# Optimization experiments

Hardware: AMD Instinct MI355X
Metric: run time of the kernel (lower is better)

## Reference

```python
import jax, jax.numpy as jnp
import numpy as np
import math

B, S, D, H, DFF = 4, 2048, 1024, 16, 4096
DK = D // 2  # 512; per-head dim = DK // H = 32
LN_EPS = 1e-3  # keras LayerNormalization default


def gelu_tanh(x):
    c = math.sqrt(2.0 / math.pi)
    return 0.5 * x * (1.0 + jnp.tanh(c * (x + 0.044715 * x * x * x)))


def layer_norm(z, g, b):
    mu = jnp.mean(z, axis=-1, keepdims=True)
    var = jnp.mean(jnp.square(z - mu), axis=-1, keepdims=True)
    return (z - mu) * jax.lax.rsqrt(var + LN_EPS) * g + b


def setup_inputs() -> dict:
    key = jax.random.key(0)
    ks = jax.random.split(key, 10)
    s = 0.02
    return {
        "x": jax.random.normal(ks[0], (B, S, D), dtype=jnp.float32),
        "mask": jnp.zeros((1, 1, S, S), dtype=jnp.float32),
        "Wq": jax.random.normal(ks[1], (D, DK), dtype=jnp.float32) * s,
        "bq": jnp.zeros((DK,), jnp.float32),
        "Wk": jax.random.normal(ks[2], (D, DK), dtype=jnp.float32) * s,
        "bk": jnp.zeros((DK,), jnp.float32),
        "Wv": jax.random.normal(ks[3], (D, DK), dtype=jnp.float32) * s,
        "bv": jnp.zeros((DK,), jnp.float32),
        "Wo": jax.random.normal(ks[4], (DK, D), dtype=jnp.float32) * s,
        "bo": jnp.zeros((D,), jnp.float32),
        "W1": jax.random.normal(ks[5], (D, DFF), dtype=jnp.float32) * s,
        "b1": jnp.zeros((DFF,), jnp.float32),
        "W2": jax.random.normal(ks[6], (DFF, D), dtype=jnp.float32) * s,
        "b2": jnp.zeros((D,), jnp.float32),
        "g1": jnp.ones((D,), jnp.float32),
        "be1": jnp.zeros((D,), jnp.float32),
        "g2": jnp.ones((D,), jnp.float32),
        "be2": jnp.zeros((D,), jnp.float32),
    }


def reference(x, mask, Wq, bq, Wk, bk, Wv, bv, Wo, bo, W1, b1, W2, b2, g1, be1, g2, be2):
    dh = DK // H
    # QKV projections: D -> DK total, split over H heads
    q = (x @ Wq + bq).reshape(B, S, H, dh).transpose(0, 2, 1, 3)  # [B,H,S,dh]
    k = (x @ Wk + bk).reshape(B, S, H, dh).transpose(0, 2, 1, 3)
    v = (x @ Wv + bv).reshape(B, S, H, dh).transpose(0, 2, 1, 3)
    # NOTE: source scales by sqrt(d_k)=sqrt(DK), not per-head dim
    scores = jnp.einsum("bhqd,bhkd->bhqk", q, k) / jnp.sqrt(jnp.asarray(DK, x.dtype))
    scores = scores + (-1e9) * mask
    w = jax.nn.softmax(scores, axis=-1)
    o = jnp.einsum("bhqk,bhkd->bhqd", w, v)  # [B,H,S,dh]
    o = o.transpose(0, 2, 1, 3).reshape(B, S, DK)
    attn_out = o @ Wo + bo  # [B,S,D]
    h1 = layer_norm(x + attn_out, g1, be1)
    # NOTE: source applies GELU AFTER the second Dense
    ff = gelu_tanh((h1 @ W1 + b1) @ W2 + b2)
    return layer_norm(h1 + ff, g2, be2)
```

## Files before the change

### kernel.cpp

```cpp
#include <hip/hip_runtime.h>

typedef unsigned short u16;
typedef unsigned int   u32;
typedef short s16x8 __attribute__((ext_vector_type(8)));
typedef float f32x4 __attribute__((ext_vector_type(4)));
typedef s16x8 __attribute__((may_alias)) s16x8_a;
typedef f32x4 __attribute__((may_alias)) f32x4_a;

#define S_LEN   2048
#define D_MODEL 1024
#define DK_DIM  512
#define DFF_DIM 4096
#define MS_ROWS 8192

__device__ __forceinline__ u16 f2bf(float f) {
  union { float f; unsigned u; } x; x.f = f;
  unsigned r = x.u + 0x7fffu + ((x.u >> 16) & 1u);
  return (u16)(r >> 16);
}
__device__ __forceinline__ float bf2f(u16 u) {
  union { unsigned u; float f; } x; x.u = ((unsigned)u) << 16; return x.f;
}

__device__ __forceinline__ void gload_lds16(const void* g, void* l) {
  __builtin_amdgcn_global_load_lds(
      (const __attribute__((address_space(1))) unsigned int*)g,
      (__attribute__((address_space(3))) unsigned int*)l, 16, 0, 0);
}


__global__ __launch_bounds__(256)
void cast_f32_bf16(const float* __restrict__ in, u16* __restrict__ out, int n) {
  for (int i = (blockIdx.x * 256 + threadIdx.x) * 4; i < n; i += gridDim.x * 256 * 4) {
    float4 f = *(const float4*)&in[i];
    ushort4 u;
    u.x = f2bf(f.x); u.y = f2bf(f.y); u.z = f2bf(f.z); u.w = f2bf(f.w);
    *(ushort4*)&out[i] = u;
  }
}

__global__ __launch_bounds__(256)
void cast_transpose_t(const float* __restrict__ W, u16* __restrict__ Wt, int K, int N) {
  __shared__ float T[64][65];
  const int k0 = blockIdx.x * 64, n0 = blockIdx.y * 64;
  const int tr = threadIdx.x >> 4;
  const int tc = (threadIdx.x & 15) * 4;
#pragma unroll
  for (int i = 0; i < 4; i++) {
    float4 v = *(const float4*)&W[(size_t)(k0 + tr + i * 16) * N + n0 + tc];
    T[tr + i * 16][tc + 0] = v.x; T[tr + i * 16][tc + 1] = v.y;
    T[tr + i * 16][tc + 2] = v.z; T[tr + i * 16][tc + 3] = v.w;
  }
  __syncthreads();
#pragma unroll
  for (int i = 0; i < 4; i++) {
    int nrow = tr + i * 16;
    ushort4 u;
    u.x = f2bf(T[tc + 0][nrow]); u.y = f2bf(T[tc + 1][nrow]);
    u.z = f2bf(T[tc + 2][nrow]); u.w = f2bf(T[tc + 3][nrow]);
    *(ushort4*)&Wt[(size_t)(n0 + nrow) * K + k0 + tc] = u;
  }
}

__global__ __launch_bounds__(256)
void fill0(float* __restrict__ p, int n) {
  int i = blockIdx.x * 256 + threadIdx.x;
  if (i < n) p[i] = 0.f;
}

__global__ __launch_bounds__(256)
void wct_reduce(const float* __restrict__ wctp, u16* __restrict__ wct) {
  int i = (blockIdx.x * 256 + threadIdx.x) * 4;
  float4 s = *(const float4*)&wctp[i];
#pragma unroll
  for (int p = 1; p < 8; p++) {
    float4 v = *(const float4*)&wctp[(size_t)p * 1048576 + i];
    s.x += v.x; s.y += v.y; s.z += v.z; s.w += v.w;
  }
  ushort4 u;
  u.x = f2bf(s.x); u.y = f2bf(s.y); u.z = f2bf(s.z); u.w = f2bf(s.w);
  *(ushort4*)&wct[i] = u;
}

__global__ __launch_bounds__(64)
void bc_make(const float* __restrict__ b1, const float* __restrict__ b2,
             const u16* __restrict__ w2t, float* __restrict__ bc) {
  int n = blockIdx.x, l = threadIdx.x;
  float s = 0.f;
  for (int d = l * 8; d < DFF_DIM; d += 64 * 8) {
    s16x8 v = *(const s16x8_a*)&w2t[(size_t)n * DFF_DIM + d];
#pragma unroll
    for (int j = 0; j < 8; j++) s += b1[d + j] * bf2f((u16)v[j]);
  }
#pragma unroll
  for (int o = 32; o > 0; o >>= 1) s += __shfl_down(s, o, 64);
  if (l == 0) bc[n] = s + b2[n];
}


template<int BM, int TBN, int OMODE>
__global__ __launch_bounds__(512, 2)
void gemm8(const u16* __restrict__ A, const u16* __restrict__ Bt,
           const float* __restrict__ b1p, const float* __restrict__ b2p,
           const float* __restrict__ b3p,
           float* __restrict__ Cf, u16* __restrict__ Cb,
           u16* __restrict__ Ck, u16* __restrict__ Cv,
           int M, int N, int K)
{
  constexpr int NF = TBN / 64;
  constexpr int MF = BM / 32;
  constexpr int MFP = MF / 4;
  constexpr int LA = BM / 128;
  constexpr int LB = TBN / 128;
  constexpr int AHROWS = BM / 2;
  constexpr int BHROWS = TBN / 2;
  constexpr int AH_U = AHROWS * 64;
  constexpr int SLOT_B0 = BM * 64;
  constexpr int BUFU = BM * 64 + TBN * 64;
  __shared__ __align__(16) u16 lds[2 * BUFU];

  const int tid = threadIdx.x;
  const int l = tid & 63, w = tid >> 6;
  const int wrow = w >> 2, wcol = w & 3;
  const int fr = l & 15, g = l >> 4;

  const int nxt = N / TBN;
  const int nwg = gridDim.x;
  const int wg = (blockIdx.x & 7) * (nwg >> 3) + (blockIdx.x >> 3);
  const int n0 = (wg % nxt) * TBN;
  const int m0 = (wg / nxt) * BM;

  const int NT = K / 64;
  const int NITER = NT / 2;

  const int srow = l >> 3;
  const int sgc  = (l & 7) ^ srow;
  auto stageA = [&](int buf, int part, int kt) {
#pragma unroll
    for (int i = 0; i < LA; i++) {
      int row = i * 64 + w * 8 + srow;
      gload_lds16(A + (size_t)(m0 + part * AHROWS + row) * K + kt * 64 + sgc * 8,
                  (void*)&lds[buf * BUFU + part * AH_U + (i * 512 + w * 64) * 8]);
    }
  };
  auto stageB = [&](int buf, int part, int kt) {
#pragma unroll
    for (int i = 0; i < LB; i++) {
      int row = i * 64 + w * 8 + srow;
      gload_lds16(Bt + (size_t)(n0 + part * BHROWS + row) * K + kt * 64 + sgc * 8,
                  (void*)&lds[buf * BUFU + SLOT_B0 + part * (TBN * 32) + (i * 512 + w * 64) * 8]);
    }
  };

  f32x4 acc[MF][NF];
#pragma unroll
  for (int m = 0; m < MF; m++)
#pragma unroll
    for (int n = 0; n < NF; n++)
#pragma unroll
      for (int r = 0; r < 4; r++) acc[m][n][r] = 0.f;
  s16x8 bfrag[NF][2];

  stageA(0, 0, 0); stageA(0, 1, 0); stageB(0, 0, 0); stageB(0, 1, 0);
  stageB(1, 0, 1); stageB(1, 1, 1);
  if (LB == 2) asm volatile("s_waitcnt vmcnt(4)" ::: "memory");
  else         asm volatile("s_waitcnt vmcnt(2)" ::: "memory");
  __builtin_amdgcn_s_barrier();

  auto phase = [&](int buf, int q, auto stager, int vm) {
    s16x8 afr[MFP][2];
    const int abase = buf * BUFU + wrow * AH_U;
#pragma unroll
    for (int f2 = 0; f2 < MFP; f2++)
#pragma unroll
      for (int kk = 0; kk < 2; kk++)
        afr[f2][kk] = *(const s16x8_a*)
            &lds[abase + ((q * MFP + f2) * 16 + fr) * 64 + (((kk * 4 + g) ^ (fr & 7)) * 8)];
    if (q == 0) {
      const int bbase = buf * BUFU + SLOT_B0 + (wcol >> 1) * (TBN * 32) + (wcol & 1) * ((TBN / 4) * 64);
#pragma unroll
      for (int n = 0; n < NF; n++)
#pragma unroll
        for (int kk = 0; kk < 2; kk++)
          bfrag[n][kk] = *(const s16x8_a*)
              &lds[bbase + (n * 16 + fr) * 64 + (((kk * 4 + g) ^ (fr & 7)) * 8)];
    }
    stager();
    if (q == 0)
      asm volatile("s_waitcnt lgkmcnt(8)" ::: "memory");
    __builtin_amdgcn_s_barrier();
    asm volatile("s_waitcnt lgkmcnt(0)" ::: "memory");
    __builtin_amdgcn_sched_barrier(0);
    __builtin_amdgcn_s_setprio(1);
#pragma unroll
    for (int f2 = 0; f2 < MFP; f2++)
#pragma unroll
      for (int n = 0; n < NF; n++)
#pragma unroll
        for (int kk = 0; kk < 2; kk++)
          acc[q * MFP + f2][n] = __builtin_amdgcn_mfma_f32_16x16x32_bf16(
              afr[f2][kk], bfrag[n][kk], acc[q * MFP + f2][n], 0, 0, 0);
    __builtin_amdgcn_s_setprio(0);
    if (vm == 0)      asm volatile("s_waitcnt vmcnt(0)" ::: "memory");
    else if (vm == 2) asm volatile("s_waitcnt vmcnt(2)" ::: "memory");
    else if (vm == 4) asm volatile("s_waitcnt vmcnt(4)" ::: "memory");
    __builtin_amdgcn_s_barrier();
  };

  for (int j = 0; j < NITER; ++j) {
    const int t1 = 2 * j + 1;
    const bool more = (j + 1 < NITER);
    phase(0, 0, [&]{ stageA(1, 0, t1); }, -1);
    phase(0, 1, [&]{ stageA(1, 1, t1); }, -1);
    phase(0, 2, [&]{ if (more) stageB(0, 0, t1 + 1); }, -1);
    phase(0, 3, [&]{ if (more) stageB(0, 1, t1 + 1); }, more ? 2 * LB : 0);
    phase(1, 0, [&]{ if (more) stageA(0, 0, t1 + 1); }, -1);
    phase(1, 1, [&]{ if (more) stageA(0, 1, t1 + 1); }, -1);
    phase(1, 2, [&]{ if (more) stageB(1, 0, t1 + 2); }, -1);
    phase(1, 3, [&]{ if (more) stageB(1, 1, t1 + 2); }, more ? 2 * LB : -1);
  }

  const int rb = m0 + wrow * AHROWS + g * 4;
  const int cb = n0 + wcol * (TBN / 4) + fr;
#pragma unroll
  for (int m = 0; m < MF; m++) {
#pragma unroll
    for (int n = 0; n < NF; n++) {
      const int col = cb + n * 16;
      const int row0 = rb + m * 16;
      if (OMODE == 0) {
        float bz = b1p[col];
#pragma unroll
        for (int r = 0; r < 4; r++)
          Cb[(size_t)(row0 + r) * N + col] = f2bf(acc[m][n][r] + bz);
      } else if (OMODE == 1) {
        float bz = b1p[col];
#pragma unroll
        for (int r = 0; r < 4; r++)
          Cf[(size_t)(row0 + r) * N + col] = acc[m][n][r] + bz;
      } else {
        if (col < 512) {
          float bz = b1p[col];
#pragma unroll
          for (int r = 0; r < 4; r++)
            Cb[(size_t)(row0 + r) * 512 + col] = f2bf(acc[m][n][r] + bz);
        } else if (col < 1024) {
          float bz = b2p[col - 512];
#pragma unroll
          for (int r = 0; r < 4; r++)
            Ck[(size_t)(row0 + r) * 512 + (col - 512)] = f2bf(acc[m][n][r] + bz);
        } else {
          float bz = b3p[col - 1024];
          const int cv = col - 1024;
          const int bb = row0 >> 11, ss = row0 & 2047;
          const int hd = cv >> 5, dd = cv & 31;
          ushort4 u4;
          u4.x = f2bf(acc[m][n][0] + bz);
          u4.y = f2bf(acc[m][n][1] + bz);
          u4.z = f2bf(acc[m][n][2] + bz);
          u4.w = f2bf(acc[m][n][3] + bz);
          *(ushort4*)&Cv[((size_t)(bb * 16 + hd) * 32 + dd) * 2048 + ss] = u4;
        }
      }
    }
  }
}


template<int OMODE, bool TRIBIAS>
__global__ __launch_bounds__(512, 4)
void gemmT(const u16* __restrict__ A, const u16* __restrict__ Bt,
           const float* __restrict__ b1p, const float* __restrict__ b2p,
           const float* __restrict__ b3p,
           float* __restrict__ Cf, u16* __restrict__ Cb,
           int M, int N, int Kblk, int lda, long partStride)
{
  __shared__ __align__(16) u16 lds[3 * 12288];

  const int tid = threadIdx.x;
  const int l = tid & 63, w = tid >> 6;
  const int wrow = w >> 2, wcol = w & 3;
  const int fr = l & 15, g = l >> 4;

  const int nxt = N >> 8;
  const int nwg = gridDim.x;
  const int wg = (blockIdx.x & 7) * (nwg >> 3) + (blockIdx.x >> 3);
  const int n0 = (wg % nxt) * 256;
  const int m0 = (wg / nxt) * 128;
  const long koff = (long)blockIdx.y * Kblk;

  const int NT = Kblk >> 5;

  const int srow = l >> 2;
  const int sck  = (l & 3) ^ ((l >> 3) & 3);
  auto stage = [&](int kt, int bi) {
    const long kb = koff + kt * 32 + sck * 8;
    gload_lds16(A + (size_t)(m0 + w * 16 + srow) * lda + kb,
                (void*)&lds[bi * 12288 + w * 512]);
    gload_lds16(Bt + (size_t)(n0 + w * 16 + srow) * lda + kb,
                (void*)&lds[bi * 12288 + 4096 + w * 512]);
    gload_lds16(Bt + (size_t)(n0 + 128 + w * 16 + srow) * lda + kb,
                (void*)&lds[bi * 12288 + 8192 + w * 512]);
  };

  f32x4 acc[4][4];
#pragma unroll
  for (int m = 0; m < 4; m++)
#pragma unroll
    for (int n = 0; n < 4; n++)
#pragma unroll
      for (int r = 0; r < 4; r++) acc[m][n][r] = 0.f;

  stage(0, 0);
  stage(1, 1);
  asm volatile("s_waitcnt vmcnt(3)" ::: "memory");
  __builtin_amdgcn_s_barrier();

  const int rsw = (g ^ ((fr >> 1) & 3)) * 8;
  int bi = 0;
  for (int t = 0; t < NT; ++t) {
    s16x8 afr[4], bfr[4];
    const int ab = bi * 12288 + fr * 32 + rsw;
#pragma unroll
    for (int m = 0; m < 4; m++)
      afr[m] = *(const s16x8_a*)&lds[ab + (wrow * 64 + m * 16) * 32];
#pragma unroll
    for (int n = 0; n < 4; n++)
      bfr[n] = *(const s16x8_a*)&lds[ab + 4096 + (wcol * 64 + n * 16) * 32];
    const bool more2 = (t + 2 < NT);
    if (more2) {
      int b2i = bi + 2; if (b2i >= 3) b2i -= 3;
      stage(t + 2, b2i);
    }
    asm volatile("s_waitcnt lgkmcnt(0)" ::: "memory");
    __builtin_amdgcn_sched_barrier(0);
    __builtin_amdgcn_s_setprio(1);
#pragma unroll
    for (int m = 0; m < 4; m++)
#pragma unroll
      for (int n = 0; n < 4; n++)
        acc[m][n] = __builtin_amdgcn_mfma_f32_16x16x32_bf16(afr[m], bfr[n], acc[m][n], 0, 0, 0);
    __builtin_amdgcn_s_setprio(0);
    if (more2)            asm volatile("s_waitcnt vmcnt(3)" ::: "memory");
    else if (t + 1 < NT)  asm volatile("s_waitcnt vmcnt(0)" ::: "memory");
    __builtin_amdgcn_s_barrier();
    bi = (bi + 1 == 3) ? 0 : bi + 1;
  }

  float* ldsf = (float*)lds;
  const bool dobias = (blockIdx.y == 0);
#pragma unroll
  for (int p = 0; p < 2; p++) {
    if (p) __syncthreads();
    const int wb = w * 2180;
#pragma unroll
    for (int j = 0; j < 2; j++)
#pragma unroll
      for (int n = 0; n < 4; n++)
#pragma unroll
        for (int r = 0; r < 4; r++)
          ldsf[wb + (j * 16 + g * 4 + r) * 68 + n * 16 + fr] = acc[2 * p + j][n][r];
    __syncthreads();
#pragma unroll
    for (int i = 0; i < 8; i++) {
      int lin = i * 512 + tid;
      int rl = lin >> 6, ch = lin & 63;
      int row_g = m0 + 32 * p + (rl & 31) + (rl >> 5) * 64;
      int colbase = n0 + ch * 4;
      const float* src = &ldsf[((rl >> 5) * 4 + (ch >> 4)) * 2180 + (rl & 31) * 68 + (ch & 15) * 4];
      f32x4 v = *(const f32x4_a*)src;
      if (dobias) {
        const float* bp;
        int cb2;
        if (TRIBIAS) {
          bp = colbase < 512 ? b1p : (colbase < 1024 ? b2p : b3p);
          cb2 = colbase & 511;
        } else { bp = b1p; cb2 = colbase; }
        float4 bz = *(const float4*)&bp[cb2];
        v[0] += bz.x; v[1] += bz.y; v[2] += bz.z; v[3] += bz.w;
      }
      if (OMODE == 1) {
        *(float4*)&Cf[(size_t)row_g * N + colbase + blockIdx.y * partStride] =
            *(float4*)&v;
      } else {
        ushort4 u;
        u.x = f2bf(v[0]); u.y = f2bf(v[1]); u.z = f2bf(v[2]); u.w = f2bf(v[3]);
        *(ushort4*)&Cb[(size_t)row_g * N + colbase] = u;
      }
    }
  }
}


__global__ __launch_bounds__(256, 4)
void flash_attn(const u16* __restrict__ q, const u16* __restrict__ k,
                const u16* __restrict__ vt, u16* __restrict__ o)
{
  __shared__ __align__(16) u16 Ks[64 * 32];
  __shared__ __align__(16) u16 Vts[32 * 72];
  __shared__ __align__(16) u32 Ps[4 * 16 * 36];
  const int tid = threadIdx.x;
  const int l = tid & 63, w = tid >> 6;
  const int fr = l & 15, g = l >> 4;
  const int fk = g * 8;
  const int bh = blockIdx.y;
  const int b = bh >> 4, head = bh & 15;
  const int s0 = blockIdx.x * 128;
  const size_t qk_base = (size_t)b * S_LEN * DK_DIM + (size_t)head * 32;
  const size_t vt_base = (size_t)bh * 32 * S_LEN;

  s16x8 qf[2];
#pragma unroll
  for (int hh = 0; hh < 2; hh++)
    qf[hh] = *(const s16x8_a*)&q[qk_base + (size_t)(s0 + w * 32 + hh * 16 + fr) * DK_DIM + fk];

  f32x4 oacc[2][2];
#pragma unroll
  for (int hh = 0; hh < 2; hh++)
#pragma unroll
    for (int nb = 0; nb < 2; nb++)
#pragma unroll
      for (int r = 0; r < 4; r++) oacc[hh][nb][r] = 0.f;
  float lsum[2] = {0.f, 0.f};

  const float kScale = 0.044194173824159216f;

  const int kc_row = w * 16 + (l >> 2);
  const int kc_col = (l & 3) * 8;
  const int vd = tid >> 3;
  const int vc = tid & 7;
  const int wbase = w * 576;

  for (int kb = 0; kb < S_LEN; kb += 64) {
    gload_lds16(&k[qk_base + (size_t)(kb + kc_row) * DK_DIM + kc_col], (void*)&Ks[w * 512]);
    {
      s16x8 vv = *(const s16x8_a*)&vt[vt_base + (size_t)vd * S_LEN + kb + vc * 8];
      *(s16x8_a*)&Vts[vd * 72 + vc * 8] = vv;
    }
    __syncthreads();

    s16x8 af[4], vf[2][2];
#pragma unroll
    for (int nb = 0; nb < 4; nb++)
      af[nb] = *(const s16x8_a*)&Ks[(nb * 16 + fr) * 32 + fk];
#pragma unroll
    for (int kk = 0; kk < 2; kk++)
#pragma unroll
      for (int nb = 0; nb < 2; nb++)
        vf[kk][nb] = *(const s16x8_a*)&Vts[(nb * 16 + fr) * 72 + kk * 32 + fk];

#pragma unroll
    for (int hh = 0; hh < 2; hh++) {
      f32x4 sc[4];
#pragma unroll
      for (int nb = 0; nb < 4; nb++) {
        f32x4 z; z[0] = 0.f; z[1] = 0.f; z[2] = 0.f; z[3] = 0.f;
        sc[nb] = __builtin_amdgcn_mfma_f32_16x16x32_bf16(af[nb], qf[hh], z, 0, 0, 0);
      }
      float ls = 0.f;
#pragma unroll
      for (int nb = 0; nb < 4; nb++)
#pragma unroll
        for (int r = 0; r < 4; r++) {
          float p = __expf(sc[nb][r] * kScale);
          sc[nb][r] = p; ls += p;
        }
      lsum[hh] += ls;
#pragma unroll
      for (int nb = 0; nb < 4; nb++) {
        u32 pk0, pk1;
        asm("v_cvt_pk_bf16_f32 %0, %1, %2" : "=v"(pk0) : "v"(sc[nb][0]), "v"(sc[nb][1]));
        asm("v_cvt_pk_bf16_f32 %0, %1, %2" : "=v"(pk1) : "v"(sc[nb][2]), "v"(sc[nb][3]));
        Ps[wbase + fr * 36 + nb * 8 + g * 2] = pk0;
        Ps[wbase + fr * 36 + nb * 8 + g * 2 + 1] = pk1;
      }
#pragma unroll
      for (int kk = 0; kk < 2; kk++) {
        s16x8 pf = *(const s16x8_a*)&Ps[wbase + fr * 36 + kk * 16 + g * 4];
#pragma unroll
        for (int nb = 0; nb < 2; nb++)
          oacc[hh][nb] = __builtin_amdgcn_mfma_f32_16x16x32_bf16(pf, vf[kk][nb], oacc[hh][nb], 0, 0, 0);
      }
    }
    __syncthreads();
  }

#pragma unroll
  for (int hh = 0; hh < 2; hh++) {
    lsum[hh] += __shfl_xor(lsum[hh], 16, 64);
    lsum[hh] += __shfl_xor(lsum[hh], 32, 64);
  }
#pragma unroll
  for (int hh = 0; hh < 2; hh++) {
    float inv[4];
#pragma unroll
    for (int r = 0; r < 4; r++)
      inv[r] = 1.0f / __shfl(lsum[hh], g * 4 + r, 64);
#pragma unroll
    for (int nb = 0; nb < 2; nb++)
#pragma unroll
      for (int r = 0; r < 4; r++) {
        int row = s0 + w * 32 + hh * 16 + g * 4 + r;
        o[qk_base + (size_t)row * DK_DIM + nb * 16 + fr] = f2bf(oacc[hh][nb][r] * inv[r]);
      }
  }
}


__global__ __launch_bounds__(256)
void ln_res(const float* __restrict__ x, const float* __restrict__ attn,
            const float* __restrict__ g, const float* __restrict__ be,
            u16* __restrict__ h1b)
{
  __shared__ float red[8];
  const int row = blockIdx.x;
  const int c4 = threadIdx.x * 4;
  const size_t bidx = (size_t)row * D_MODEL + c4;
  float4 xa = *(const float4*)&x[bidx];
  float4 ab = *(const float4*)&attn[bidx];
  float z0 = xa.x + ab.x, z1 = xa.y + ab.y, z2 = xa.z + ab.z, z3 = xa.w + ab.w;
  float s = z0 + z1 + z2 + z3;
  float s2 = z0 * z0 + z1 * z1 + z2 * z2 + z3 * z3;
#pragma unroll
  for (int o = 32; o > 0; o >>= 1) { s += __shfl_down(s, o, 64); s2 += __shfl_down(s2, o, 64); }
  const int w = threadIdx.x >> 6;
  if ((threadIdx.x & 63) == 0) { red[w] = s; red[4 + w] = s2; }
  __syncthreads();
  s  = red[0] + red[1] + red[2] + red[3];
  s2 = red[4] + red[5] + red[6] + red[7];
  float mu = s * (1.f / D_MODEL);
  float var = s2 * (1.f / D_MODEL) - mu * mu;
  float rs = rsqrtf(var + 1e-3f);
  float4 gv = *(const float4*)&g[c4];
  float4 bv = *(const float4*)&be[c4];
  ushort4 hb;
  hb.x = f2bf((z0 - mu) * rs * gv.x + bv.x);
  hb.y = f2bf((z1 - mu) * rs * gv.y + bv.y);
  hb.z = f2bf((z2 - mu) * rs * gv.z + bv.z);
  hb.w = f2bf((z3 - mu) * rs * gv.w + bv.w);
  *(ushort4*)&h1b[bidx] = hb;
}

__device__ __forceinline__ float gelu_t(float u) {
  float t = tanhf(0.7978845608028654f * (u + 0.044715f * u * u * u));
  return 0.5f * u * (1.f + t);
}

__global__ __launch_bounds__(256)
void ln_gelu(float* __restrict__ io, const u16* __restrict__ h1b,
             const float* __restrict__ g, const float* __restrict__ be)
{
  __shared__ float red[8];
  const int row = blockIdx.x;
  const int c4 = threadIdx.x * 4;
  const size_t bidx = (size_t)row * D_MODEL + c4;
  float4 fa = *(const float4*)&io[bidx];
  ushort4 hb = *(const ushort4*)&h1b[bidx];
  float z0 = bf2f(hb.x) + gelu_t(fa.x);
  float z1 = bf2f(hb.y) + gelu_t(fa.y);
  float z2 = bf2f(hb.z) + gelu_t(fa.z);
  float z3 = bf2f(hb.w) + gelu_t(fa.w);
  float s = z0 + z1 + z2 + z3;
  float s2 = z0 * z0 + z1 * z1 + z2 * z2 + z3 * z3;
#pragma unroll
  for (int o = 32; o > 0; o >>= 1) { s += __shfl_down(s, o, 64); s2 += __shfl_down(s2, o, 64); }
  const int w = threadIdx.x >> 6;
  if ((threadIdx.x & 63) == 0) { red[w] = s; red[4 + w] = s2; }
  __syncthreads();
  s  = red[0] + red[1] + red[2] + red[3];
  s2 = red[4] + red[5] + red[6] + red[7];
  float mu = s * (1.f / D_MODEL);
  float var = s2 * (1.f / D_MODEL) - mu * mu;
  float rs = rsqrtf(var + 1e-3f);
  float4 gv = *(const float4*)&g[c4];
  float4 bv = *(const float4*)&be[c4];
  float4 ov;
  ov.x = (z0 - mu) * rs * gv.x + bv.x;
  ov.y = (z1 - mu) * rs * gv.y + bv.y;
  ov.z = (z2 - mu) * rs * gv.z + bv.z;
  ov.w = (z3 - mu) * rs * gv.w + bv.w;
  *(float4*)&io[bidx] = ov;
}


extern "C" void kernel_launch(void* const* d_in, const int* in_sizes, int n_in,
                              void* d_out, int out_size, void* d_ws, size_t ws_size,
                              hipStream_t stream)
{
  const float* x   = (const float*)d_in[0];
  const float* Wq  = (const float*)d_in[2];
  const float* bq  = (const float*)d_in[3];
  const float* Wk  = (const float*)d_in[4];
  const float* bk  = (const float*)d_in[5];
  const float* Wv  = (const float*)d_in[6];
  const float* bv  = (const float*)d_in[7];
  const float* Wo  = (const float*)d_in[8];
  const float* bo  = (const float*)d_in[9];
  const float* W1  = (const float*)d_in[10];
  const float* b1  = (const float*)d_in[11];
  const float* W2  = (const float*)d_in[12];
  const float* b2  = (const float*)d_in[13];
  const float* g1  = (const float*)d_in[14];
  const float* be1 = (const float*)d_in[15];
  const float* g2  = (const float*)d_in[16];
  const float* be2 = (const float*)d_in[17];
  float* out = (float*)d_out;

  char* ws = (char*)d_ws;
  size_t off = 0;
  auto alloc = [&](size_t bytes) -> void* {
    void* p = ws + off;
    off += (bytes + 255) & ~(size_t)255;
    return p;
  };
  u16*   xb    = (u16*)  alloc((size_t)MS_ROWS * D_MODEL * 2);
  u16*   qb    = (u16*)  alloc((size_t)MS_ROWS * DK_DIM * 2);
  u16*   kbuf  = (u16*)  alloc((size_t)MS_ROWS * DK_DIM * 2);
  u16*   vtb   = (u16*)  alloc((size_t)64 * 32 * S_LEN * 2);
  float* attn  = (float*)alloc((size_t)MS_ROWS * D_MODEL * 4);
  u16*   obuf  = (u16*)  alloc((size_t)MS_ROWS * DK_DIM * 2);
  u16*   wqkvt = (u16*)  alloc((size_t)3 * DK_DIM * D_MODEL * 2);
  u16*   wot   = (u16*)  alloc((size_t)DK_DIM * D_MODEL * 2);
  u16*   w1c   = (u16*)  alloc((size_t)D_MODEL * DFF_DIM * 2);
  u16*   w2t   = (u16*)  alloc((size_t)DFF_DIM * D_MODEL * 2);
  u16*   wct   = (u16*)  alloc((size_t)D_MODEL * D_MODEL * 2);
  u16*   h1b   = (u16*)  alloc((size_t)MS_ROWS * D_MODEL * 2);
  float* bzero = (float*)alloc(1024 * 4);
  float* bc    = (float*)alloc(1024 * 4);
  float* wctp  = attn;

  cast_f32_bf16<<<2048, 256, 0, stream>>>(x, xb, MS_ROWS * D_MODEL);
  cast_f32_bf16<<<2048, 256, 0, stream>>>(W1, w1c, D_MODEL * DFF_DIM);
  cast_transpose_t<<<dim3(D_MODEL / 64, DK_DIM / 64),  256, 0, stream>>>(Wq, wqkvt, D_MODEL, DK_DIM);
  cast_transpose_t<<<dim3(D_MODEL / 64, DK_DIM / 64),  256, 0, stream>>>(Wk, wqkvt + (size_t)DK_DIM * D_MODEL, D_MODEL, DK_DIM);
  cast_transpose_t<<<dim3(D_MODEL / 64, DK_DIM / 64),  256, 0, stream>>>(Wv, wqkvt + (size_t)2 * DK_DIM * D_MODEL, D_MODEL, DK_DIM);
  cast_transpose_t<<<dim3(DK_DIM / 64, D_MODEL / 64),  256, 0, stream>>>(Wo, wot, DK_DIM, D_MODEL);
  cast_transpose_t<<<dim3(DFF_DIM / 64, D_MODEL / 64), 256, 0, stream>>>(W2, w2t, DFF_DIM, D_MODEL);
  fill0<<<4, 256, 0, stream>>>(bzero, 1024);

  gemmT<1, false><<<dim3((1024 / 128) * (1024 / 256), 8), 512, 0, stream>>>(
      w2t, w1c, bzero, nullptr, nullptr, wctp, nullptr,
      1024, 1024, DFF_DIM / 8, DFF_DIM, (long)(1024 * 1024));
  wct_reduce<<<1024, 256, 0, stream>>>(wctp, wct);
  bc_make<<<1024, 64, 0, stream>>>(b1, b2, w2t, bc);

  gemm8<128, 256, 2><<<(MS_ROWS / 128) * (1536 / 256), 512, 0, stream>>>(
      xb, wqkvt, bq, bk, bv, nullptr, qb, kbuf, vtb, MS_ROWS, 1536, D_MODEL);

  flash_attn<<<dim3(S_LEN / 128, 64), 256, 0, stream>>>(qb, kbuf, vtb, obuf);

  gemm8<128, 256, 1><<<(MS_ROWS / 128) * (D_MODEL / 256), 512, 0, stream>>>(
      obuf, wot, bo, bo, bo, attn, nullptr, nullptr, nullptr, MS_ROWS, D_MODEL, DK_DIM);

  ln_res<<<MS_ROWS, 256, 0, stream>>>(x, attn, g1, be1, h1b);

  gemm8<128, 256, 1><<<(MS_ROWS / 128) * (D_MODEL / 256), 512, 0, stream>>>(
      h1b, wct, bc, bc, bc, out, nullptr, nullptr, nullptr, MS_ROWS, D_MODEL, D_MODEL);

  ln_gelu<<<MS_ROWS, 256, 0, stream>>>(out, h1b, g2, be2);
}
```

Measured before the change: 244.1 us.

## Double-buffer K/V tiles in flash attention and fold softmax scale into Q

```diff
diff --git a/kernel.cpp b/kernel.cpp
--- a/kernel.cpp
+++ b/kernel.cpp
@@ -4,8 +4,10 @@
 typedef unsigned int   u32;
 typedef short s16x8 __attribute__((ext_vector_type(8)));
 typedef float f32x4 __attribute__((ext_vector_type(4)));
+typedef u32   u32x2 __attribute__((ext_vector_type(2)));
 typedef s16x8 __attribute__((may_alias)) s16x8_a;
 typedef f32x4 __attribute__((may_alias)) f32x4_a;
+typedef u32x2 __attribute__((may_alias)) u32x2_a;
 
 #define S_LEN   2048
 #define D_MODEL 1024
@@ -243,7 +245,8 @@
           float bz = b1p[col];
 #pragma unroll
           for (int r = 0; r < 4; r++)
-            Cb[(size_t)(row0 + r) * 512 + col] = f2bf(acc[m][n][r] + bz);
+            Cb[(size_t)(row0 + r) * 512 + col] =
+                f2bf((acc[m][n][r] + bz) * 0.044194173824159216f);
         } else if (col < 1024) {
           float bz = b2p[col - 512];
 #pragma unroll
@@ -396,9 +399,9 @@
 void flash_attn(const u16* __restrict__ q, const u16* __restrict__ k,
                 const u16* __restrict__ vt, u16* __restrict__ o)
 {
-  __shared__ __align__(16) u16 Ks[64 * 32];
-  __shared__ __align__(16) u16 Vts[32 * 72];
-  __shared__ __align__(16) u32 Ps[4 * 16 * 36];
+  __shared__ __align__(16) u16 Ks[2][64 * 32];
+  __shared__ __align__(16) u16 Vts[2][32 * 72];
+  __shared__ __align__(16) u32 Ps[4][16 * 36];
   const int tid = threadIdx.x;
   const int l = tid & 63, w = tid >> 6;
   const int fr = l & 15, g = l >> 4;
@@ -423,31 +426,40 @@
       for (int r = 0; r < 4; r++) oacc[hh][nb][r] = 0.f;
   float lsum[2] = {0.f, 0.f};
 
-  const float kScale = 0.044194173824159216f;
-
   const int kc_row = w * 16 + (l >> 2);
   const int kc_col = (l & 3) * 8;
   const int vd = tid >> 3;
   const int vc = tid & 7;
-  const int wbase = w * 576;
-
-  for (int kb = 0; kb < S_LEN; kb += 64) {
-    gload_lds16(&k[qk_base + (size_t)(kb + kc_row) * DK_DIM + kc_col], (void*)&Ks[w * 512]);
-    {
-      s16x8 vv = *(const s16x8_a*)&vt[vt_base + (size_t)vd * S_LEN + kb + vc * 8];
-      *(s16x8_a*)&Vts[vd * 72 + vc * 8] = vv;
-    }
-    __syncthreads();
+
+  const int NTILE = S_LEN / 64;
+
+  gload_lds16(&k[qk_base + (size_t)(0 + kc_row) * DK_DIM + kc_col], (void*)&Ks[0][w * 512]);
+  {
+    s16x8 vv0 = *(const s16x8_a*)&vt[vt_base + (size_t)vd * S_LEN + 0 + vc * 8];
+    asm volatile("s_waitcnt vmcnt(0)" ::: "memory");
+    *(s16x8_a*)&Vts[0][vd * 72 + vc * 8] = vv0;
+  }
+  __syncthreads();
+
+  for (int t = 0; t < NTILE; t++) {
+    const int cur = t & 1, nx = cur ^ 1;
+    const bool more = (t + 1 < NTILE);
+    s16x8 vv;
+    if (more) {
+      gload_lds16(&k[qk_base + (size_t)((t + 1) * 64 + kc_row) * DK_DIM + kc_col],
+                  (void*)&Ks[nx][w * 512]);
+      vv = *(const s16x8_a*)&vt[vt_base + (size_t)vd * S_LEN + (t + 1) * 64 + vc * 8];
+    }
 
     s16x8 af[4], vf[2][2];
 #pragma unroll
     for (int nb = 0; nb < 4; nb++)
-      af[nb] = *(const s16x8_a*)&Ks[(nb * 16 + fr) * 32 + fk];
+      af[nb] = *(const s16x8_a*)&Ks[cur][(nb * 16 + fr) * 32 + fk];
 #pragma unroll
     for (int kk = 0; kk < 2; kk++)
 #pragma unroll
       for (int nb = 0; nb < 2; nb++)
-        vf[kk][nb] = *(const s16x8_a*)&Vts[(nb * 16 + fr) * 72 + kk * 32 + fk];
+        vf[kk][nb] = *(const s16x8_a*)&Vts[cur][(nb * 16 + fr) * 72 + kk * 32 + fk];
 
 #pragma unroll
     for (int hh = 0; hh < 2; hh++) {
@@ -462,7 +474,7 @@
       for (int nb = 0; nb < 4; nb++)
 #pragma unroll
         for (int r = 0; r < 4; r++) {
-          float p = __expf(sc[nb][r] * kScale);
+          float p = __expf(sc[nb][r]);
           sc[nb][r] = p; ls += p;
         }
       lsum[hh] += ls;
@@ -471,16 +483,21 @@
         u32 pk0, pk1;
         asm("v_cvt_pk_bf16_f32 %0, %1, %2" : "=v"(pk0) : "v"(sc[nb][0]), "v"(sc[nb][1]));
         asm("v_cvt_pk_bf16_f32 %0, %1, %2" : "=v"(pk1) : "v"(sc[nb][2]), "v"(sc[nb][3]));
-        Ps[wbase + fr * 36 + nb * 8 + g * 2] = pk0;
-        Ps[wbase + fr * 36 + nb * 8 + g * 2 + 1] = pk1;
+        u32x2 pr; pr.x = pk0; pr.y = pk1;
+        *(u32x2_a*)&Ps[w][fr * 36 + nb * 8 + g * 2] = pr;
       }
 #pragma unroll
       for (int kk = 0; kk < 2; kk++) {
-        s16x8 pf = *(const s16x8_a*)&Ps[wbase + fr * 36 + kk * 16 + g * 4];
+        s16x8 pf = *(const s16x8_a*)&Ps[w][fr * 36 + kk * 16 + g * 4];
 #pragma unroll
         for (int nb = 0; nb < 2; nb++)
           oacc[hh][nb] = __builtin_amdgcn_mfma_f32_16x16x32_bf16(pf, vf[kk][nb], oacc[hh][nb], 0, 0, 0);
       }
+    }
+
+    if (more) {
+      asm volatile("s_waitcnt vmcnt(0)" ::: "memory");
+      *(s16x8_a*)&Vts[nx][vd * 72 + vc * 8] = vv;
     }
     __syncthreads();
   }
```

Measured after the change: 237.5 us. 1.03x faster.
